# Kernel tuning notes

Measured on AMD Instinct MI355X. Metric: run time of the kernel, lower is better.

Reference implementation:

```python
import jax, jax.numpy as jnp
import numpy as np

N = 100000          # number of road-network nodes
E = 640000          # number of directed edges (sparse adjacency nnz)
HID = 128           # hidden_dims = lane(16)+type(32)+length(16)+node(64)
N_LAYERS = 3        # hparams.baseline_gat_layer


def setup_inputs() -> dict:
    key = jax.random.key(0)
    ks = jax.random.split(key, 12)
    inp = {
        'node_feature': jax.random.randint(ks[0], (N,), 0, 100000),
        'type_feature': jax.random.randint(ks[1], (N,), 0, 20),
        'length_feature': jax.random.randint(ks[2], (N,), 0, 100),
        'lane_feature': jax.random.randint(ks[3], (N,), 0, 10),
        'adj_src': jax.random.randint(ks[4], (E,), 0, N),
        'adj_dst': jax.random.randint(ks[5], (E,), 0, N),
        'adj_val': jax.random.uniform(ks[6], (E,), dtype=jnp.float32),
        # learned parameters
        'node_emb': jax.random.normal(ks[7], (100000, 64), dtype=jnp.float32) * 0.02,
        'type_emb': jax.random.normal(ks[8], (20, 32), dtype=jnp.float32) * 0.02,
        'length_emb': jax.random.normal(ks[9], (100, 16), dtype=jnp.float32) * 0.02,
        'lane_emb': jax.random.normal(ks[10], (10, 16), dtype=jnp.float32) * 0.02,
        'W': jax.random.normal(ks[11], (HID, HID), dtype=jnp.float32) / np.sqrt(HID),
        'b': jnp.zeros((HID,), dtype=jnp.float32),
    }
    return inp


def spgcn_layer(x, W, b, adj_src, adj_dst, adj_val):
    # GCN layer: out = spmm(adj, x @ W) + b, adj given as COO edge list
    support = x @ W                                # [N, HID]
    msg = support[adj_src] * adj_val[:, None]      # gather + scale, [E, HID]
    agg = jax.ops.segment_sum(msg, adj_dst, num_segments=N)  # scatter-add
    return agg + b


def reference(node_feature, type_feature, length_feature, lane_feature,
              adj_src, adj_dst, adj_val,
              node_emb, type_emb, length_emb, lane_emb, W, b):
    # embedding lookups + concat: [lane, type, length, node] -> [N, HID]
    raw_feat = jnp.concatenate([
        lane_emb[lane_feature],
        type_emb[type_feature],
        length_emb[length_feature],
        node_emb[node_feature],
    ], axis=1)
    # repeated propagation with the SAME shared SPGCN layer weights
    for _ in range(N_LAYERS):
        raw_feat = spgcn_layer(raw_feat, W, b, adj_src, adj_dst, adj_val)
    return raw_feat
```

## Files before the change

### kernel.cpp

```cpp
#include <hip/hip_runtime.h>
#include <hip/hip_bf16.h>

typedef __hip_bfloat16 bf16;
typedef unsigned short ushort_t;
typedef __attribute__((ext_vector_type(8))) short short8;
typedef __attribute__((ext_vector_type(4))) float f32x4;

#define NN 100000
#define NE 640000
#define HD 128
#define NB 391
#define EMB_U 6250
#define PREP_U 64
#define CNT_U 391
#define PH0_U (EMB_U + PREP_U + CNT_U)
#define HIST_U 2500
#define GEMM_U 782
#define AGG_U 12500
#define D_U 391
#define LDA 136


__device__ __forceinline__ float bf2f(ushort_t u) {
    unsigned v = (unsigned)u << 16;
    return __builtin_bit_cast(float, v);
}
__device__ __forceinline__ ushort_t f2bf(float f) {
    bf16 h = __float2bfloat16(f);
    return *(ushort_t*)&h;
}

struct P {
    const int *nodef, *typef, *lenf, *lanef, *adj_src, *adj_dst;
    const float *adj_val, *node_emb, *type_emb, *len_emb, *lane_emb, *W, *bias;
    ushort_t *Xa, *Xb, *Wt, *w3t;
    float *bw, *bw2, *d, *d2;
    int *cnt, *offs, *pos, *bsum;
    int2 *epack;
    float *outf;
};


__global__ __launch_bounds__(256) void phase0_k(P p) {
    const int v = blockIdx.x;
    const int tid = threadIdx.x;
    if (v < EMB_U) {
        const int idx = v * 256 + tid;
        const int i = idx >> 4;
        const int c = (idx & 15) * 8;
        const float* tbl; size_t base;
        if (c < 16)      { tbl = p.lane_emb; base = (size_t)p.lanef[i] * 16 + c; }
        else if (c < 48) { tbl = p.type_emb; base = (size_t)p.typef[i] * 32 + (c - 16); }
        else if (c < 64) { tbl = p.len_emb;  base = (size_t)p.lenf[i]  * 16 + (c - 48); }
        else             { tbl = p.node_emb; base = (size_t)p.nodef[i] * 64 + (c - 64); }
        const float4 f0 = *(const float4*)(tbl + base);
        const float4 f1 = *(const float4*)(tbl + base + 4);
        ushort_t u8[8] = { f2bf(f0.x), f2bf(f0.y), f2bf(f0.z), f2bf(f0.w),
                           f2bf(f1.x), f2bf(f1.y), f2bf(f1.z), f2bf(f1.w) };
        *(uint4*)(p.Xa + (size_t)i * HD + c) = *(uint4*)u8;
    } else if (v < EMB_U + PREP_U) {
        const int idx = (v - EMB_U) * 256 + tid;
        const int n = idx >> 7, k = idx & 127;
        p.Wt[idx] = f2bf(p.W[(size_t)k * HD + n]);
    } else {
        const int idx = (v - EMB_U - PREP_U) * 256 + tid;
        if (idx < NN) p.cnt[idx] = 0;
    }
}

__global__ __launch_bounds__(256) void wchain_k(P p) {
    __shared__ ushort_t WtL[HD * HD];
    __shared__ ushort_t W2t[HD * HD];
    const int tid = threadIdx.x;
    for (int i = tid; i < HD * HD / 8; i += 256)
        *(uint4*)&WtL[i * 8] = *(const uint4*)&p.Wt[i * 8];
    __syncthreads();

    const int w = tid >> 6;
    const int ln = tid & 15;
    const int quad = (tid >> 4) & 3;
    const int koff = quad * 8;
    const f32x4 zero = {0.f, 0.f, 0.f, 0.f};

    short8 bfrg[2][4];
#pragma unroll
    for (int nt = 0; nt < 2; ++nt)
#pragma unroll
        for (int kc = 0; kc < 4; ++kc)
            bfrg[nt][kc] = *(const short8*)&WtL[(w * 32 + nt * 16 + ln) * HD + kc * 32 + koff];

#pragma unroll
    for (int mt = 0; mt < 8; ++mt) {
        const int m = mt * 16 + ln;
        short8 afrg[4];
#pragma unroll
        for (int kc = 0; kc < 4; ++kc) {
            ushort_t a[8];
#pragma unroll
            for (int j = 0; j < 8; ++j)
                a[j] = WtL[(kc * 32 + koff + j) * HD + m];
            afrg[kc] = *(short8*)a;
        }
        f32x4 acc[2] = {zero, zero};
#pragma unroll
        for (int nt = 0; nt < 2; ++nt)
#pragma unroll
            for (int kc = 0; kc < 4; ++kc)
                acc[nt] = __builtin_amdgcn_mfma_f32_16x16x32_bf16(
                        afrg[kc], bfrg[nt][kc], acc[nt], 0, 0, 0);
#pragma unroll
        for (int nt = 0; nt < 2; ++nt)
#pragma unroll
            for (int reg = 0; reg < 4; ++reg) {
                const int col = w * 32 + nt * 16 + ln;
                const int row = mt * 16 + quad * 4 + reg;
                W2t[col * HD + row] = f2bf(acc[nt][reg]);
            }
    }
    __syncthreads();

#pragma unroll
    for (int mt = 0; mt < 8; ++mt) {
        const int m = mt * 16 + ln;
        short8 afrg[4];
#pragma unroll
        for (int kc = 0; kc < 4; ++kc) {
            ushort_t a[8];
#pragma unroll
            for (int j = 0; j < 8; ++j)
                a[j] = W2t[(kc * 32 + koff + j) * HD + m];
            afrg[kc] = *(short8*)a;
        }
        f32x4 acc[2] = {zero, zero};
#pragma unroll
        for (int nt = 0; nt < 2; ++nt)
#pragma unroll
            for (int kc = 0; kc < 4; ++kc)
                acc[nt] = __builtin_amdgcn_mfma_f32_16x16x32_bf16(
                        afrg[kc], bfrg[nt][kc], acc[nt], 0, 0, 0);
#pragma unroll
        for (int nt = 0; nt < 2; ++nt)
#pragma unroll
            for (int reg = 0; reg < 4; ++reg) {
                const int col = w * 32 + nt * 16 + ln;
                const int row = mt * 16 + quad * 4 + reg;
                p.w3t[col * HD + row] = f2bf(acc[nt][reg]);
            }
    }
    __syncthreads();

    float* bwS = (float*)W2t;
    if (tid < HD) {
        float s = 0.f;
        for (int k = 0; k < HD; ++k) s += p.bias[k] * bf2f(WtL[tid * HD + k]);
        bwS[tid] = s;
        p.bw[tid] = s;
    }
    __syncthreads();
    if (tid < HD) {
        float s = 0.f;
        for (int k = 0; k < HD; ++k) s += bwS[k] * bf2f(WtL[tid * HD + k]);
        p.bw2[tid] = s;
    }
}


__global__ __launch_bounds__(256) void hist_k(P p) {
    const int e = blockIdx.x * 256 + threadIdx.x;
    atomicAdd(&p.cnt[p.adj_dst[e]], 1);
}

__global__ __launch_bounds__(256) void scan1_k(P p) {
    __shared__ int s[256];
    const int tid = threadIdx.x;
    const int idx = blockIdx.x * 256 + tid;
    s[tid] = (idx < NN) ? p.cnt[idx] : 0;
    __syncthreads();
    for (int o = 128; o; o >>= 1) {
        if (tid < o) s[tid] += s[tid + o];
        __syncthreads();
    }
    if (tid == 0) p.bsum[blockIdx.x] = s[0];
}

__global__ __launch_bounds__(256) void scan3_k(P p) {
    __shared__ int s[256];
    const int b = blockIdx.x;
    const int tid = threadIdx.x;
    int acc = 0;
    for (int i = tid; i < b; i += 256) acc += p.bsum[i];
    s[tid] = acc;
    __syncthreads();
    for (int o = 128; o; o >>= 1) {
        if (tid < o) s[tid] += s[tid + o];
        __syncthreads();
    }
    const int boffv = s[0];
    __syncthreads();
    const int idx = b * 256 + tid;
    int v = (idx < NN) ? p.cnt[idx] : 0;
    s[tid] = v;
    __syncthreads();
    for (int o = 1; o < 256; o <<= 1) {
        int x = (tid >= o) ? s[tid - o] : 0;
        __syncthreads();
        s[tid] += x;
        __syncthreads();
    }
    const int excl = s[tid] - v + boffv;
    if (idx <= NN) {
        p.offs[idx] = excl;
        if (idx < NN) p.pos[idx] = excl;
    }
}

__global__ __launch_bounds__(256) void position_k(P p) {
    const int e = blockIdx.x * 256 + threadIdx.x;
    const int d = p.adj_dst[e];
    const int slot = atomicAdd(&p.pos[d], 1);
    int2 pk;
    pk.x = p.adj_src[e];
    pk.y = __float_as_int(p.adj_val[e]);
    p.epack[slot] = pk;
}

__global__ __launch_bounds__(256) void agg_k(P p, const ushort_t* __restrict__ Xin,
                                             ushort_t* __restrict__ Xout, int aux) {
    if (blockIdx.x >= AGG_U) {
        const int node = (blockIdx.x - AGG_U) * 256 + threadIdx.x;
        if (node < NN) {
            const int lo = p.offs[node], hi = p.offs[node + 1];
            float s = 0.f;
            if (aux == 1) {
                for (int j = lo; j < hi; ++j) s += __int_as_float(p.epack[j].y);
                p.d[node] = s;
            } else {
                for (int j = lo; j < hi; ++j) {
                    const int2 e = p.epack[j];
                    s += __int_as_float(e.y) * p.d[e.x];
                }
                p.d2[node] = s;
            }
        }
        return;
    }
    const int node = blockIdx.x * 8 + (threadIdx.x >> 5);
    const int lane = threadIdx.x & 31;
    const int c = lane * 4;
    const int lo = p.offs[node];
    const int hi = p.offs[node + 1];
    float4 a0 = {0,0,0,0}, a1 = {0,0,0,0}, a2 = {0,0,0,0}, a3 = {0,0,0,0};
    int j = lo;
    for (; j + 3 < hi; j += 4) {
        const int2 e0 = p.epack[j], e1 = p.epack[j + 1];
        const int2 e2 = p.epack[j + 2], e3 = p.epack[j + 3];
        const ushort4 u0 = *(const ushort4*)(Xin + (size_t)e0.x * HD + c);
        const ushort4 u1 = *(const ushort4*)(Xin + (size_t)e1.x * HD + c);
        const ushort4 u2 = *(const ushort4*)(Xin + (size_t)e2.x * HD + c);
        const ushort4 u3 = *(const ushort4*)(Xin + (size_t)e3.x * HD + c);
        const float v0 = __int_as_float(e0.y), v1 = __int_as_float(e1.y);
        const float v2 = __int_as_float(e2.y), v3 = __int_as_float(e3.y);
        a0.x += bf2f(u0.x)*v0; a0.y += bf2f(u0.y)*v0; a0.z += bf2f(u0.z)*v0; a0.w += bf2f(u0.w)*v0;
        a1.x += bf2f(u1.x)*v1; a1.y += bf2f(u1.y)*v1; a1.z += bf2f(u1.z)*v1; a1.w += bf2f(u1.w)*v1;
        a2.x += bf2f(u2.x)*v2; a2.y += bf2f(u2.y)*v2; a2.z += bf2f(u2.z)*v2; a2.w += bf2f(u2.w)*v2;
        a3.x += bf2f(u3.x)*v3; a3.y += bf2f(u3.y)*v3; a3.z += bf2f(u3.z)*v3; a3.w += bf2f(u3.w)*v3;
    }
    for (; j < hi; ++j) {
        const int2 e0 = p.epack[j];
        const float v0 = __int_as_float(e0.y);
        const ushort4 u0 = *(const ushort4*)(Xin + (size_t)e0.x * HD + c);
        a0.x += bf2f(u0.x)*v0; a0.y += bf2f(u0.y)*v0; a0.z += bf2f(u0.z)*v0; a0.w += bf2f(u0.w)*v0;
    }
    float4 acc;
    acc.x = (a0.x + a1.x) + (a2.x + a3.x);
    acc.y = (a0.y + a1.y) + (a2.y + a3.y);
    acc.z = (a0.z + a1.z) + (a2.z + a3.z);
    acc.w = (a0.w + a1.w) + (a2.w + a3.w);
    ushort4 u; u.x = f2bf(acc.x); u.y = f2bf(acc.y); u.z = f2bf(acc.z); u.w = f2bf(acc.w);
    *(ushort4*)(Xout + (size_t)node * HD + c) = u;
}

__global__ __launch_bounds__(256) void gemmf_k(P p, const ushort_t* __restrict__ X3) {
    __shared__ ushort_t Xs[128 * LDA];
    const int tid = threadIdx.x;
    const int row0 = blockIdx.x * 128;

#pragma unroll
    for (int i = 0; i < 8; ++i) {
        int chunk = i * 256 + tid;
        int m = chunk >> 4;
        int c8 = (chunk & 15) * 8;
        int gm = row0 + m;
        if (gm >= NN) gm = NN - 1;
        *(uint4*)&Xs[m * LDA + c8] = *(const uint4*)&X3[(size_t)gm * HD + c8];
    }

    const int w = tid >> 6;
    const int ln = tid & 15;
    const int quad = (tid >> 4) & 3;
    const int koff = quad * 8;
    const int col0 = w * 32 + ln;
    const int col1 = col0 + 16;

    short8 bfrg[2][4];
#pragma unroll
    for (int nt = 0; nt < 2; ++nt)
#pragma unroll
        for (int kc = 0; kc < 4; ++kc)
            bfrg[nt][kc] = *(const short8*)&p.w3t[(size_t)(w * 32 + nt * 16 + ln) * HD + kc * 32 + koff];

    const float bwc0 = p.bw[col0],  bwc1 = p.bw[col1];
    const float bw2c0 = p.bw2[col0], bw2c1 = p.bw2[col1];
    const float bc0 = p.bias[col0], bc1 = p.bias[col1];

    __syncthreads();

    const f32x4 zero = {0.f, 0.f, 0.f, 0.f};
#pragma unroll
    for (int mt = 0; mt < 8; ++mt) {
        short8 afrg[4];
#pragma unroll
        for (int kc = 0; kc < 4; ++kc)
            afrg[kc] = *(const short8*)&Xs[(mt * 16 + ln) * LDA + kc * 32 + koff];
        f32x4 acc[2] = {zero, zero};
#pragma unroll
        for (int nt = 0; nt < 2; ++nt)
#pragma unroll
            for (int kc = 0; kc < 4; ++kc)
                acc[nt] = __builtin_amdgcn_mfma_f32_16x16x32_bf16(
                        afrg[kc], bfrg[nt][kc], acc[nt], 0, 0, 0);
#pragma unroll
        for (int reg = 0; reg < 4; ++reg) {
            const int gm = row0 + mt * 16 + quad * 4 + reg;
            if (gm < NN) {
                const float dg = p.d[gm], d2g = p.d2[gm];
                p.outf[(size_t)gm * HD + col0] = acc[0][reg] + d2g * bw2c0 + dg * bwc0 + bc0;
                p.outf[(size_t)gm * HD + col1] = acc[1][reg] + d2g * bw2c1 + dg * bwc1 + bc1;
            }
        }
    }
}

extern "C" void kernel_launch(void* const* d_in, const int* in_sizes, int n_in,
                              void* d_out, int out_size, void* d_ws, size_t ws_size,
                              hipStream_t stream) {
    P p;
    p.nodef    = (const int*)d_in[0];
    p.typef    = (const int*)d_in[1];
    p.lenf     = (const int*)d_in[2];
    p.lanef    = (const int*)d_in[3];
    p.adj_src  = (const int*)d_in[4];
    p.adj_dst  = (const int*)d_in[5];
    p.adj_val  = (const float*)d_in[6];
    p.node_emb = (const float*)d_in[7];
    p.type_emb = (const float*)d_in[8];
    p.len_emb  = (const float*)d_in[9];
    p.lane_emb = (const float*)d_in[10];
    p.W        = (const float*)d_in[11];
    p.bias     = (const float*)d_in[12];
    p.outf     = (float*)d_out;

    const size_t xbytes = (size_t)NN * HD * 2;
    char* wp = (char*)d_ws;
    p.Xa    = (ushort_t*)wp; wp += xbytes;
    p.Xb    = (ushort_t*)wp; wp += xbytes;
    p.cnt   = (int*)wp;      wp += (size_t)NN * 4;
    p.offs  = (int*)wp;      wp += 400016;
    p.pos   = (int*)wp;      wp += (size_t)NN * 4;
    p.epack = (int2*)wp;     wp += (size_t)NE * 8;
    p.Wt    = (ushort_t*)wp; wp += 32768;
    p.w3t   = (ushort_t*)wp; wp += 32768;
    p.bw    = (float*)wp;    wp += 512;
    p.bw2   = (float*)wp;    wp += 512;
    p.d     = (float*)wp;    wp += (size_t)NN * 4;
    p.d2    = (float*)wp;    wp += (size_t)NN * 4;
    p.bsum  = (int*)wp;      wp += 1600;

    phase0_k<<<PH0_U, 256, 0, stream>>>(p);
    wchain_k<<<1, 256, 0, stream>>>(p);
    hist_k<<<HIST_U, 256, 0, stream>>>(p);
    scan1_k<<<NB, 256, 0, stream>>>(p);
    scan3_k<<<NB, 256, 0, stream>>>(p);
    position_k<<<HIST_U, 256, 0, stream>>>(p);
    agg_k<<<AGG_U + D_U, 256, 0, stream>>>(p, p.Xa, p.Xb, 1);
    agg_k<<<AGG_U + D_U, 256, 0, stream>>>(p, p.Xb, p.Xa, 2);
    agg_k<<<AGG_U, 256, 0, stream>>>(p, p.Xa, p.Xb, 0);
    gemmf_k<<<GEMM_U, 256, 0, stream>>>(p, p.Xb);
}
```

Before: 323.6 us.

## Fuse weight chain into histogram, compute degree via atomics, fuse last aggregation into GEMM

The single-block weight-chain kernel is merged into the histogram kernel as an extra block, and the intermediate W^2 now goes to global memory instead of LDS. The per-node value sums are accumulated with float atomics during the histogram, which removes one aggregation launch. The third aggregation is folded into the GEMM kernel's tile load so X3 never round-trips through global memory. The aggregation is also widened to 16 lanes × 8 bf16 per node. In exchange, the fused GEMM does its gather with low parallelism per block (each 16-lane group handles 8 rows serially), and the float atomic order makes the degree sums nondeterministic.

```diff
diff --git a/kernel.cpp b/kernel.cpp
--- a/kernel.cpp
+++ b/kernel.cpp
@@ -16,7 +16,7 @@
 #define PH0_U (EMB_U + PREP_U + CNT_U)
 #define HIST_U 2500
 #define GEMM_U 782
-#define AGG_U 12500
+#define AGG_U 6250
 #define D_U 391
 #define LDA 136
 
@@ -33,7 +33,7 @@
 struct P {
     const int *nodef, *typef, *lenf, *lanef, *adj_src, *adj_dst;
     const float *adj_val, *node_emb, *type_emb, *len_emb, *lane_emb, *W, *bias;
-    ushort_t *Xa, *Xb, *Wt, *w3t;
+    ushort_t *Xa, *Xb, *Wt, *w2t, *w3t;
     float *bw, *bw2, *d, *d2;
     int *cnt, *offs, *pos, *bsum;
     int2 *epack;
@@ -64,14 +64,21 @@
         p.Wt[idx] = f2bf(p.W[(size_t)k * HD + n]);
     } else {
         const int idx = (v - EMB_U - PREP_U) * 256 + tid;
-        if (idx < NN) p.cnt[idx] = 0;
-    }
-}
-
-__global__ __launch_bounds__(256) void wchain_k(P p) {
+        if (idx < NN) { p.cnt[idx] = 0; p.d[idx] = 0.f; }
+    }
+}
+
+__global__ __launch_bounds__(256) void histw_k(P p) {
+    const int tid = threadIdx.x;
+    if (blockIdx.x < HIST_U) {
+        const int e = blockIdx.x * 256 + tid;
+        const int dst = p.adj_dst[e];
+        atomicAdd(&p.cnt[dst], 1);
+        atomicAdd(&p.d[dst], p.adj_val[e]);
+        return;
+    }
     __shared__ ushort_t WtL[HD * HD];
-    __shared__ ushort_t W2t[HD * HD];
-    const int tid = threadIdx.x;
+    __shared__ float bwS[HD];
     for (int i = tid; i < HD * HD / 8; i += 256)
         *(uint4*)&WtL[i * 8] = *(const uint4*)&p.Wt[i * 8];
     __syncthreads();
@@ -114,7 +121,7 @@
             for (int reg = 0; reg < 4; ++reg) {
                 const int col = w * 32 + nt * 16 + ln;
                 const int row = mt * 16 + quad * 4 + reg;
-                W2t[col * HD + row] = f2bf(acc[nt][reg]);
+                p.w2t[col * HD + row] = f2bf(acc[nt][reg]);
             }
     }
     __syncthreads();
@@ -128,7 +135,7 @@
             ushort_t a[8];
 #pragma unroll
             for (int j = 0; j < 8; ++j)
-                a[j] = W2t[(kc * 32 + koff + j) * HD + m];
+                a[j] = p.w2t[(kc * 32 + koff + j) * HD + m];
             afrg[kc] = *(short8*)a;
         }
         f32x4 acc[2] = {zero, zero};
@@ -149,7 +156,6 @@
     }
     __syncthreads();
 
-    float* bwS = (float*)W2t;
     if (tid < HD) {
         float s = 0.f;
         for (int k = 0; k < HD; ++k) s += p.bias[k] * bf2f(WtL[tid * HD + k]);
@@ -164,11 +170,6 @@
     }
 }
 
-
-__global__ __launch_bounds__(256) void hist_k(P p) {
-    const int e = blockIdx.x * 256 + threadIdx.x;
-    atomicAdd(&p.cnt[p.adj_dst[e]], 1);
-}
 
 __global__ __launch_bounds__(256) void scan1_k(P p) {
     __shared__ int s[256];
@@ -225,74 +226,108 @@
 }
 
 __global__ __launch_bounds__(256) void agg_k(P p, const ushort_t* __restrict__ Xin,
-                                             ushort_t* __restrict__ Xout, int aux) {
+                                             ushort_t* __restrict__ Xout) {
     if (blockIdx.x >= AGG_U) {
         const int node = (blockIdx.x - AGG_U) * 256 + threadIdx.x;
         if (node < NN) {
             const int lo = p.offs[node], hi = p.offs[node + 1];
             float s = 0.f;
-            if (aux == 1) {
-                for (int j = lo; j < hi; ++j) s += __int_as_float(p.epack[j].y);
-                p.d[node] = s;
-            } else {
-                for (int j = lo; j < hi; ++j) {
-                    const int2 e = p.epack[j];
-                    s += __int_as_float(e.y) * p.d[e.x];
-                }
-                p.d2[node] = s;
+            for (int j = lo; j < hi; ++j) {
+                const int2 e = p.epack[j];
+                s += __int_as_float(e.y) * p.d[e.x];
             }
+            p.d2[node] = s;
         }
         return;
     }
-    const int node = blockIdx.x * 8 + (threadIdx.x >> 5);
-    const int lane = threadIdx.x & 31;
-    const int c = lane * 4;
+    const int node = blockIdx.x * 16 + (threadIdx.x >> 4);
+    const int lane = threadIdx.x & 15;
+    const int c = lane * 8;
     const int lo = p.offs[node];
     const int hi = p.offs[node + 1];
-    float4 a0 = {0,0,0,0}, a1 = {0,0,0,0}, a2 = {0,0,0,0}, a3 = {0,0,0,0};
+    float a0[8], a1[8], a2[8], a3[8];
+#pragma unroll
+    for (int k = 0; k < 8; ++k) { a0[k] = a1[k] = a2[k] = a3[k] = 0.f; }
     int j = lo;
     for (; j + 3 < hi; j += 4) {
         const int2 e0 = p.epack[j], e1 = p.epack[j + 1];
         const int2 e2 = p.epack[j + 2], e3 = p.epack[j + 3];
-        const ushort4 u0 = *(const ushort4*)(Xin + (size_t)e0.x * HD + c);
-        const ushort4 u1 = *(const ushort4*)(Xin + (size_t)e1.x * HD + c);
-        const ushort4 u2 = *(const ushort4*)(Xin + (size_t)e2.x * HD + c);
-        const ushort4 u3 = *(const ushort4*)(Xin + (size_t)e3.x * HD + c);
+        const short8 u0 = *(const short8*)(Xin + (size_t)e0.x * HD + c);
+        const short8 u1 = *(const short8*)(Xin + (size_t)e1.x * HD + c);
+        const short8 u2 = *(const short8*)(Xin + (size_t)e2.x * HD + c);
+        const short8 u3 = *(const short8*)(Xin + (size_t)e3.x * HD + c);
         const float v0 = __int_as_float(e0.y), v1 = __int_as_float(e1.y);
         const float v2 = __int_as_float(e2.y), v3 = __int_as_float(e3.y);
-        a0.x += bf2f(u0.x)*v0; a0.y += bf2f(u0.y)*v0; a0.z += bf2f(u0.z)*v0; a0.w += bf2f(u0.w)*v0;
-        a1.x += bf2f(u1.x)*v1; a1.y += bf2f(u1.y)*v1; a1.z += bf2f(u1.z)*v1; a1.w += bf2f(u1.w)*v1;
-        a2.x += bf2f(u2.x)*v2; a2.y += bf2f(u2.y)*v2; a2.z += bf2f(u2.z)*v2; a2.w += bf2f(u2.w)*v2;
-        a3.x += bf2f(u3.x)*v3; a3.y += bf2f(u3.y)*v3; a3.z += bf2f(u3.z)*v3; a3.w += bf2f(u3.w)*v3;
+#pragma unroll
+        for (int k = 0; k < 8; ++k) {
+            a0[k] += bf2f((ushort_t)u0[k]) * v0;
+            a1[k] += bf2f((ushort_t)u1[k]) * v1;
+            a2[k] += bf2f((ushort_t)u2[k]) * v2;
+            a3[k] += bf2f((ushort_t)u3[k]) * v3;
+        }
     }
     for (; j < hi; ++j) {
         const int2 e0 = p.epack[j];
         const float v0 = __int_as_float(e0.y);
-        const ushort4 u0 = *(const ushort4*)(Xin + (size_t)e0.x * HD + c);
-        a0.x += bf2f(u0.x)*v0; a0.y += bf2f(u0.y)*v0; a0.z += bf2f(u0.z)*v0; a0.w += bf2f(u0.w)*v0;
-    }
-    float4 acc;
-    acc.x = (a0.x + a1.x) + (a2.x + a3.x);
-    acc.y = (a0.y + a1.y) + (a2.y + a3.y);
-    acc.z = (a0.z + a1.z) + (a2.z + a3.z);
-    acc.w = (a0.w + a1.w) + (a2.w + a3.w);
-    ushort4 u; u.x = f2bf(acc.x); u.y = f2bf(acc.y); u.z = f2bf(acc.z); u.w = f2bf(acc.w);
-    *(ushort4*)(Xout + (size_t)node * HD + c) = u;
-}
-
-__global__ __launch_bounds__(256) void gemmf_k(P p, const ushort_t* __restrict__ X3) {
+        const short8 u0 = *(const short8*)(Xin + (size_t)e0.x * HD + c);
+#pragma unroll
+        for (int k = 0; k < 8; ++k) a0[k] += bf2f((ushort_t)u0[k]) * v0;
+    }
+    ushort_t u8[8];
+#pragma unroll
+    for (int k = 0; k < 8; ++k) u8[k] = f2bf((a0[k] + a1[k]) + (a2[k] + a3[k]));
+    *(uint4*)(Xout + (size_t)node * HD + c) = *(uint4*)u8;
+}
+
+__global__ __launch_bounds__(256) void gemmf_k(P p, const ushort_t* __restrict__ X2) {
     __shared__ ushort_t Xs[128 * LDA];
     const int tid = threadIdx.x;
     const int row0 = blockIdx.x * 128;
 
-#pragma unroll
-    for (int i = 0; i < 8; ++i) {
-        int chunk = i * 256 + tid;
-        int m = chunk >> 4;
-        int c8 = (chunk & 15) * 8;
-        int gm = row0 + m;
-        if (gm >= NN) gm = NN - 1;
-        *(uint4*)&Xs[m * LDA + c8] = *(const uint4*)&X3[(size_t)gm * HD + c8];
+    {
+        const int g = tid >> 4;
+        const int lane = tid & 15;
+        const int c = lane * 8;
+        for (int mi = 0; mi < 8; ++mi) {
+            const int m = g * 8 + mi;
+            const int gm = row0 + m;
+            float a0[8], a1[8], a2[8], a3[8];
+#pragma unroll
+            for (int k = 0; k < 8; ++k) { a0[k] = a1[k] = a2[k] = a3[k] = 0.f; }
+            if (gm < NN) {
+                const int lo = p.offs[gm];
+                const int hi = p.offs[gm + 1];
+                int j = lo;
+                for (; j + 3 < hi; j += 4) {
+                    const int2 e0 = p.epack[j], e1 = p.epack[j + 1];
+                    const int2 e2 = p.epack[j + 2], e3 = p.epack[j + 3];
+                    const short8 u0 = *(const short8*)(X2 + (size_t)e0.x * HD + c);
+                    const short8 u1 = *(const short8*)(X2 + (size_t)e1.x * HD + c);
+                    const short8 u2 = *(const short8*)(X2 + (size_t)e2.x * HD + c);
+                    const short8 u3 = *(const short8*)(X2 + (size_t)e3.x * HD + c);
+                    const float v0 = __int_as_float(e0.y), v1 = __int_as_float(e1.y);
+                    const float v2 = __int_as_float(e2.y), v3 = __int_as_float(e3.y);
+#pragma unroll
+                    for (int k = 0; k < 8; ++k) {
+                        a0[k] += bf2f((ushort_t)u0[k]) * v0;
+                        a1[k] += bf2f((ushort_t)u1[k]) * v1;
+                        a2[k] += bf2f((ushort_t)u2[k]) * v2;
+                        a3[k] += bf2f((ushort_t)u3[k]) * v3;
+                    }
+                }
+                for (; j < hi; ++j) {
+                    const int2 e0 = p.epack[j];
+                    const float v0 = __int_as_float(e0.y);
+                    const short8 u0 = *(const short8*)(X2 + (size_t)e0.x * HD + c);
+#pragma unroll
+                    for (int k = 0; k < 8; ++k) a0[k] += bf2f((ushort_t)u0[k]) * v0;
+                }
+            }
+            ushort_t u8[8];
+#pragma unroll
+            for (int k = 0; k < 8; ++k) u8[k] = f2bf((a0[k] + a1[k]) + (a2[k] + a3[k]));
+            *(uint4*)&Xs[m * LDA + c] = *(uint4*)u8;
+        }
     }
 
     const int w = tid >> 6;
@@ -369,6 +404,7 @@
     p.pos   = (int*)wp;      wp += (size_t)NN * 4;
     p.epack = (int2*)wp;     wp += (size_t)NE * 8;
     p.Wt    = (ushort_t*)wp; wp += 32768;
+    p.w2t   = (ushort_t*)wp; wp += 32768;
     p.w3t   = (ushort_t*)wp; wp += 32768;
     p.bw    = (float*)wp;    wp += 512;
     p.bw2   = (float*)wp;    wp += 512;
@@ -377,13 +413,11 @@
     p.bsum  = (int*)wp;      wp += 1600;
 
     phase0_k<<<PH0_U, 256, 0, stream>>>(p);
-    wchain_k<<<1, 256, 0, stream>>>(p);
-    hist_k<<<HIST_U, 256, 0, stream>>>(p);
+    histw_k<<<HIST_U + 1, 256, 0, stream>>>(p);
     scan1_k<<<NB, 256, 0, stream>>>(p);
     scan3_k<<<NB, 256, 0, stream>>>(p);
     position_k<<<HIST_U, 256, 0, stream>>>(p);
-    agg_k<<<AGG_U + D_U, 256, 0, stream>>>(p, p.Xa, p.Xb, 1);
-    agg_k<<<AGG_U + D_U, 256, 0, stream>>>(p, p.Xb, p.Xa, 2);
-    agg_k<<<AGG_U, 256, 0, stream>>>(p, p.Xa, p.Xb, 0);
-    gemmf_k<<<GEMM_U, 256, 0, stream>>>(p, p.Xb);
-}
+    agg_k<<<AGG_U + D_U, 256, 0, stream>>>(p, p.Xa, p.Xb);
+    agg_k<<<AGG_U, 256, 0, stream>>>(p, p.Xb, p.Xa);
+    gemmf_k<<<GEMM_U, 256, 0, stream>>>(p, p.Xa);
+}
```

New measurement: 341.8 us. 1.06x slower.
